# Optimization experiments

Measured on AMD Instinct MI355X. Metric: run time of the kernel, lower is better.

The kernel has to match this reference:

```python
import jax, jax.numpy as jnp
import numpy as np
from jax.scipy.special import logsumexp

REG = 1.0
N_ITER = 50  # fixed Sinkhorn iterations (log-domain, stabilized)


def setup_inputs() -> dict:
    key = jax.random.key(0)
    k1, k2 = jax.random.split(key)
    source = jax.random.normal(k1, (8192, 256), dtype=jnp.float32)
    target = jax.random.normal(k2, (8192, 256), dtype=jnp.float32)
    return {"source": source, "target": target}


def _sinkhorn_value(x, y, reg):
    # squared euclidean cost matrix [n, m]
    M = (jnp.sum(x * x, axis=1)[:, None]
         + jnp.sum(y * y, axis=1)[None, :]
         - 2.0 * (x @ y.T))
    n, m = M.shape
    loga = -jnp.log(jnp.float32(n))  # uniform weights
    logb = -jnp.log(jnp.float32(m))
    Mr = M / reg

    def step(fg, _):
        f, g = fg
        # f_i = -reg * logsumexp_j((g_j - M_ij)/reg + log b_j)
        f = -reg * logsumexp(g[None, :] / reg - Mr + logb, axis=1)
        g = -reg * logsumexp(f[:, None] / reg - Mr + loga, axis=0)
        return (f, g), None

    f0 = jnp.zeros((n,), dtype=M.dtype)
    g0 = jnp.zeros((m,), dtype=M.dtype)
    (f, g), _ = jax.lax.scan(step, (f0, g0), None, length=N_ITER)

    # log P_ij = (f_i + g_j - M_ij)/reg + log a_i + log b_j
    logP = (f[:, None] + g[None, :]) / reg - Mr + (loga + logb)
    P = jnp.exp(logP)
    value_linear = jnp.sum(P * M)
    # KL(P || a x b) entropic term (reg_type='KL' default in POT)
    kl = jnp.sum(P * (logP - loga - logb))
    return value_linear + reg * kl


def reference(source, target):
    value = _sinkhorn_value(source, target, REG)
    return jnp.sqrt(value)
```

## Files before the change

### kernel.cpp

```cpp
#include <hip/hip_runtime.h>

#define N 8192
#define DK 256
#define LOG2E 1.4426950408889634f
#define LN2   0.6931471805599453f
#define ZS    2.5f
#define QS    1.1541560327f
#define BIAS  320.0f

typedef unsigned short u16;
typedef u16   ushort8 __attribute__((ext_vector_type(8)));
typedef __bf16 bf16x8 __attribute__((ext_vector_type(8)));
typedef float  f32x4  __attribute__((ext_vector_type(4)));

__device__ __forceinline__ u16 f2bf(float f){
  unsigned u = __builtin_bit_cast(unsigned, f);
  return (u16)((u + 0x7fffu + ((u >> 16) & 1u)) >> 16);
}
__device__ __forceinline__ float ex2(float x){
  float r; asm("v_exp_f32 %0, %1" : "=v"(r) : "v"(x)); return r;
}
__device__ __forceinline__ float lg2(float x){
  float r; asm("v_log_f32 %0, %1" : "=v"(r) : "v"(x)); return r;
}
__device__ __forceinline__ float cub0(unsigned u){ float r; asm("v_cvt_f32_ubyte0 %0, %1":"=v"(r):"v"(u)); return r; }
__device__ __forceinline__ float cub1(unsigned u){ float r; asm("v_cvt_f32_ubyte1 %0, %1":"=v"(r):"v"(u)); return r; }
__device__ __forceinline__ float cub2(unsigned u){ float r; asm("v_cvt_f32_ubyte2 %0, %1":"=v"(r):"v"(u)); return r; }
__device__ __forceinline__ float cub3(unsigned u){ float r; asm("v_cvt_f32_ubyte3 %0, %1":"=v"(r):"v"(u)); return r; }

__device__ __forceinline__ float quad(unsigned u, float4 gv, float M){
  float t0 = __builtin_fmaf(cub0(u), ZS, gv.x - M);
  float t1 = __builtin_fmaf(cub1(u), ZS, gv.y - M);
  float t2 = __builtin_fmaf(cub2(u), ZS, gv.z - M);
  float t3 = __builtin_fmaf(cub3(u), ZS, gv.w - M);
  return (ex2(t0) + ex2(t1)) + (ex2(t2) + ex2(t3));
}

__global__ __launch_bounds__(256) void prep_k(const float* __restrict__ x, const float* __restrict__ y,
                                              u16* __restrict__ xb, u16* __restrict__ yb,
                                              float* __restrict__ x2, float* __restrict__ y2,
                                              float* __restrict__ gts){
  const int w = threadIdx.x >> 6, l = threadIdx.x & 63;
  const int r = blockIdx.x * 4 + w;
  const bool isx = r < N;
  const int rr = isx ? r : r - N;
  const float* src = (isx ? x : y) + (size_t)rr * DK;
  float4 v = *(const float4*)(src + l * 4);
  ushort4 bv;
  bv.x = f2bf(v.x); bv.y = f2bf(v.y); bv.z = f2bf(v.z); bv.w = f2bf(v.w);
  *(ushort4*)((isx ? xb : yb) + (size_t)rr * DK + l * 4) = bv;
  float p = v.x*v.x + v.y*v.y + v.z*v.z + v.w*v.w;
  #pragma unroll
  for (int off = 32; off > 0; off >>= 1) p += __shfl_down(p, off);
  if (l == 0){
    if (isx) x2[rr] = p;
    else { y2[rr] = p; gts[rr] = -p * LOG2E - BIAS; }
  }
}

__global__ __launch_bounds__(256) void gemm_k(const u16* __restrict__ xb, const u16* __restrict__ yb,
                                              unsigned char* __restrict__ zq,
                                              unsigned char* __restrict__ zqT){
  __shared__ __align__(16) u16 As[128 * 72];
  __shared__ __align__(16) u16 Bs[128 * 72];
  const int t = threadIdx.x;
  const int w = t >> 6, l = t & 63;
  const int wm = w >> 1, wn = w & 1;
  const int brow = blockIdx.y * 128, bcol = blockIdx.x * 128;
  const int tr = t >> 3, tc = t & 7;
  f32x4 acc[4][4] = {};
  for (int ks = 0; ks < 4; ++ks){
    #pragma unroll
    for (int rr = 0; rr < 4; ++rr){
      const int row = tr + rr * 32;
      *(ushort8*)&As[row * 72 + tc * 8] = *(const ushort8*)&xb[(size_t)(brow + row) * DK + ks * 64 + tc * 8];
      *(ushort8*)&Bs[row * 72 + tc * 8] = *(const ushort8*)&yb[(size_t)(bcol + row) * DK + ks * 64 + tc * 8];
    }
    __syncthreads();
    #pragma unroll
    for (int kk = 0; kk < 2; ++kk){
      bf16x8 av[4], bv[4];
      #pragma unroll
      for (int mi = 0; mi < 4; ++mi){
        const int ar = wm * 64 + mi * 16 + (l & 15);
        av[mi] = __builtin_bit_cast(bf16x8, *(const ushort8*)&As[ar * 72 + kk * 32 + (l >> 4) * 8]);
      }
      #pragma unroll
      for (int ni = 0; ni < 4; ++ni){
        const int br = wn * 64 + ni * 16 + (l & 15);
        bv[ni] = __builtin_bit_cast(bf16x8, *(const ushort8*)&Bs[br * 72 + kk * 32 + (l >> 4) * 8]);
      }
      #pragma unroll
      for (int mi = 0; mi < 4; ++mi)
        #pragma unroll
        for (int ni = 0; ni < 4; ++ni)
          acc[mi][ni] = __builtin_amdgcn_mfma_f32_16x16x32_bf16(av[mi], bv[ni], acc[mi][ni], 0, 0, 0);
    }
    __syncthreads();
  }
  unsigned char* Cs = (unsigned char*)As;
  unsigned char* Ct = (unsigned char*)Bs;
  #pragma unroll
  for (int mi = 0; mi < 4; ++mi){
    const int rowb = wm * 64 + mi * 16 + (l >> 4) * 4;
    #pragma unroll
    for (int ni = 0; ni < 4; ++ni){
      const int col = wn * 64 + ni * 16 + (l & 15);
      unsigned pk = 0;
      #pragma unroll
      for (int rr = 0; rr < 4; ++rr){
        float q = fminf(fmaxf(acc[mi][ni][rr] * QS, -127.f), 127.f);
        unsigned b = (unsigned)((int)__builtin_rintf(q) + 128) & 255u;
        Cs[(rowb + rr) * 128 + col] = (unsigned char)b;
        pk |= b << (8 * rr);
      }
      *(unsigned*)(Ct + col * 144 + rowb) = pk;
    }
  }
  __syncthreads();
  const int trow0 = t >> 3, kseg = t & 7;
  #pragma unroll
  for (int ii = 0; ii < 4; ++ii){
    const int row = trow0 + ii * 32;
    int4 v = *(const int4*)(Cs + row * 128 + kseg * 16);
    *(int4*)(zq + (size_t)(brow + row) * N + bcol + kseg * 16) = v;
    int4 vt = *(const int4*)(Ct + row * 144 + kseg * 16);
    *(int4*)(zqT + (size_t)(bcol + row) * N + brow + kseg * 16) = vt;
  }
}

__global__ __launch_bounds__(256) void sweept_k(const unsigned char* __restrict__ z,
                                                const float* __restrict__ din,
                                                float* __restrict__ dout,
                                                float* __restrict__ pmax_out){
  const int w = threadIdx.x >> 6, l = threadIdx.x & 63;
  const int i = blockIdx.x * 4 + w;
  const unsigned char* zr = z + (size_t)i * N + l * 16;
  float m = -1e30f, s = 0.f;
  uint4 zA = *(const uint4*)(zr);
  #pragma unroll
  for (int it = 0; it < 8; ++it){
    uint4 zB = zA;
    if (it < 7) zB = *(const uint4*)(zr + (it + 1) * 1024);
    const float* gp = din + it * 1024 + l * 16;
    const float4 g0 = *(const float4*)(gp);
    const float4 g1 = *(const float4*)(gp + 4);
    const float4 g2 = *(const float4*)(gp + 8);
    const float4 g3 = *(const float4*)(gp + 12);
    float tt[16];
    tt[0]  = __builtin_fmaf(cub0(zA.x), ZS, g0.x);
    tt[1]  = __builtin_fmaf(cub1(zA.x), ZS, g0.y);
    tt[2]  = __builtin_fmaf(cub2(zA.x), ZS, g0.z);
    tt[3]  = __builtin_fmaf(cub3(zA.x), ZS, g0.w);
    tt[4]  = __builtin_fmaf(cub0(zA.y), ZS, g1.x);
    tt[5]  = __builtin_fmaf(cub1(zA.y), ZS, g1.y);
    tt[6]  = __builtin_fmaf(cub2(zA.y), ZS, g1.z);
    tt[7]  = __builtin_fmaf(cub3(zA.y), ZS, g1.w);
    tt[8]  = __builtin_fmaf(cub0(zA.z), ZS, g2.x);
    tt[9]  = __builtin_fmaf(cub1(zA.z), ZS, g2.y);
    tt[10] = __builtin_fmaf(cub2(zA.z), ZS, g2.z);
    tt[11] = __builtin_fmaf(cub3(zA.z), ZS, g2.w);
    tt[12] = __builtin_fmaf(cub0(zA.w), ZS, g3.x);
    tt[13] = __builtin_fmaf(cub1(zA.w), ZS, g3.y);
    tt[14] = __builtin_fmaf(cub2(zA.w), ZS, g3.z);
    tt[15] = __builtin_fmaf(cub3(zA.w), ZS, g3.w);
    float a0 = fmaxf(tt[0], tt[1]),  a1 = fmaxf(tt[2], tt[3]);
    float a2 = fmaxf(tt[4], tt[5]),  a3 = fmaxf(tt[6], tt[7]);
    float a4 = fmaxf(tt[8], tt[9]),  a5 = fmaxf(tt[10], tt[11]);
    float a6 = fmaxf(tt[12], tt[13]), a7 = fmaxf(tt[14], tt[15]);
    float b0 = fmaxf(a0, a1), b1 = fmaxf(a2, a3), b2 = fmaxf(a4, a5), b3 = fmaxf(a6, a7);
    float nm = fmaxf(fmaxf(fmaxf(b0, b1), fmaxf(b2, b3)), m);
    float s0 = ex2(tt[0] - nm) + ex2(tt[1] - nm) + ex2(tt[2] - nm) + ex2(tt[3] - nm)
             + ex2(tt[4] - nm) + ex2(tt[5] - nm) + ex2(tt[6] - nm) + ex2(tt[7] - nm);
    float s1 = ex2(tt[8] - nm) + ex2(tt[9] - nm) + ex2(tt[10] - nm) + ex2(tt[11] - nm)
             + ex2(tt[12] - nm) + ex2(tt[13] - nm) + ex2(tt[14] - nm) + ex2(tt[15] - nm);
    s = __builtin_fmaf(s, ex2(m - nm), s0 + s1);
    m = nm;
    zA = zB;
  }
  #pragma unroll
  for (int off = 32; off > 0; off >>= 1){
    float om = __shfl_down(m, off);
    float os = __shfl_down(s, off);
    float nm = fmaxf(m, om);
    s = __builtin_fmaf(s, ex2(m - nm), os * ex2(om - nm));
    m = nm;
  }
  if (l == 0){
    float lse2 = m + lg2(s);
    dout[i] = 13.0f - lse2 - BIAS;
    pmax_out[i] = lse2;
  }
}

template<int MODE>
__global__ __launch_bounds__(256) void sweepn_k(const unsigned char* __restrict__ z,
                                                const float* __restrict__ din,
                                                float* __restrict__ dout,
                                                const float* __restrict__ pmax_in,
                                                float* __restrict__ pmax_out,
                                                const float* __restrict__ fprev,
                                                const float* __restrict__ x2,
                                                float* __restrict__ contrib){
  __shared__ __align__(16) float gl[8192];
  const int t = threadIdx.x;
  #pragma unroll
  for (int i = 0; i < 8; ++i){
    const int idx = (t + i * 256) * 4;
    *(float4*)(gl + idx) = *(const float4*)(din + idx);
  }
  __syncthreads();
  const int w = t >> 6, l = t & 63;
  const int r0 = blockIdx.x * 8 + w * 2;
  const unsigned char* zr = z + (size_t)r0 * N + l * 16;
  const float M0 = pmax_in[r0], M1 = pmax_in[r0 + 1];
  float s0 = 0.f, s1 = 0.f;
  #pragma unroll 2
  for (int it = 0; it < 8; ++it){
    const uint4 a = *(const uint4*)(zr + it * 1024);
    const uint4 b = *(const uint4*)(zr + N + it * 1024);
    const int cb = it * 1024 + l * 16;
    {
      const float4 gv = *(const float4*)(gl + cb);
      s0 += quad(a.x, gv, M0); s1 += quad(b.x, gv, M1);
    }
    {
      const float4 gv = *(const float4*)(gl + cb + 4);
      s0 += quad(a.y, gv, M0); s1 += quad(b.y, gv, M1);
    }
    {
      const float4 gv = *(const float4*)(gl + cb + 8);
      s0 += quad(a.z, gv, M0); s1 += quad(b.z, gv, M1);
    }
    {
      const float4 gv = *(const float4*)(gl + cb + 12);
      s0 += quad(a.w, gv, M0); s1 += quad(b.w, gv, M1);
    }
  }
  #pragma unroll
  for (int off = 32; off > 0; off >>= 1){
    s0 += __shfl_down(s0, off);
    s1 += __shfl_down(s1, off);
  }
  if (l == 0){
    const float lse0 = M0 + lg2(s0);
    const float lse1 = M1 + lg2(s1);
    if (MODE == 0){
      dout[r0]     = 13.0f - lse0 - BIAS;
      dout[r0 + 1] = 13.0f - lse1 - BIAS;
      pmax_out[r0]     = lse0;
      pmax_out[r0 + 1] = lse1;
    } else {
      const float f0 = fprev[r0] + BIAS;
      const float f1 = fprev[r0 + 1] + BIAS;
      contrib[r0]     = (f0 * LN2 + x2[r0])     * ex2(f0 + lse0 - 26.0f);
      contrib[r0 + 1] = (f1 * LN2 + x2[r0 + 1]) * ex2(f1 + lse1 - 26.0f);
    }
  }
}

__global__ __launch_bounds__(256) void finish_k(const float* __restrict__ contrib,
                                                const float* __restrict__ gts,
                                                const float* __restrict__ y2,
                                                float* __restrict__ out){
  __shared__ float s1[256], s2[256];
  const int t = threadIdx.x;
  float a = 0.f, b = 0.f;
  for (int j = t; j < N; j += 256){ a += contrib[j]; b += (gts[j] + BIAS) * LN2 + y2[j]; }
  s1[t] = a; s2[t] = b; __syncthreads();
  for (int st = 128; st > 0; st >>= 1){
    if (t < st){ s1[t] += s1[t + st]; s2[t] += s2[t + st]; }
    __syncthreads();
  }
  if (t == 0) out[0] = sqrtf(s1[0] + s2[0] * (1.0f / (float)N));
}

extern "C" void kernel_launch(void* const* d_in, const int* in_sizes, int n_in,
                              void* d_out, int out_size, void* d_ws, size_t ws_size,
                              hipStream_t stream){
  const float* x = (const float*)d_in[0];
  const float* y = (const float*)d_in[1];
  float* out = (float*)d_out;
  char* ws = (char*)d_ws;

  unsigned char* zq  = (unsigned char*)(ws);
  unsigned char* zqT = (unsigned char*)(ws + 67108864);
  u16*   xb      = (u16*)  (ws + 134217728);
  u16*   yb      = (u16*)  (ws + 138412032);
  float* x2      = (float*)(ws + 142606336);
  float* y2      = (float*)(ws + 142639104);
  float* fts     = (float*)(ws + 142671872);
  float* gts     = (float*)(ws + 142704640);
  float* contrib = (float*)(ws + 142737408);
  float* pmaxF   = (float*)(ws + 142770176);
  float* pmaxG   = (float*)(ws + 142802944);

  prep_k<<<4096, 256, 0, stream>>>(x, y, xb, yb, x2, y2, gts);
  gemm_k<<<dim3(64, 64), 256, 0, stream>>>(xb, yb, zq, zqT);
  for (int it = 0; it < 2; ++it){
    sweept_k<<<2048, 256, 0, stream>>>(zq,  gts, fts, pmaxF);
    sweept_k<<<2048, 256, 0, stream>>>(zqT, fts, gts, pmaxG);
  }
  for (int s = 4; s < 100; ++s){
    if ((s & 1) == 0)
      sweepn_k<0><<<1024, 256, 0, stream>>>(zq,  gts, fts, pmaxF, pmaxF,
                                            nullptr, nullptr, nullptr);
    else
      sweepn_k<0><<<1024, 256, 0, stream>>>(zqT, fts, gts, pmaxG, pmaxG,
                                            nullptr, nullptr, nullptr);
  }
  sweepn_k<1><<<1024, 256, 0, stream>>>(zq, gts, nullptr, pmaxF, nullptr,
                                        fts, x2, contrib);
  finish_k<<<1, 256, 0, stream>>>(contrib, gts, y2, out);
}
```

Baseline: 1.708 ms.

## Fuse all Sinkhorn sweeps into one persistent cooperative kernel with grid sync

Replaces about 100 separate sweep kernel launches plus the value and finish kernels with one cooperative persistent kernel of 256 blocks × 512 threads. It uses grid.sync between half-iterations and stages the dual vector in LDS on each step. This removes per-launch overhead and the tail idle time between dependent launches. In exchange it adds grid-wide barrier cost, lowers parallelism from 1024 blocks to 256, and each block now handles 32 rows. The old multi-kernel path stays as a fallback if the cooperative launch fails.

```diff
diff --git a/kernel.cpp b/kernel.cpp
--- a/kernel.cpp
+++ b/kernel.cpp
@@ -1,4 +1,7 @@
 #include <hip/hip_runtime.h>
+#include <hip/hip_cooperative_groups.h>
+
+namespace cg = cooperative_groups;
 
 #define N 8192
 #define DK 256
@@ -34,6 +37,48 @@
   float t2 = __builtin_fmaf(cub2(u), ZS, gv.z - M);
   float t3 = __builtin_fmaf(cub3(u), ZS, gv.w - M);
   return (ex2(t0) + ex2(t1)) + (ex2(t2) + ex2(t3));
+}
+__device__ __forceinline__ float pm16(const uint4 a, const float* gp, float M){
+  const float4 g0 = *(const float4*)(gp);
+  const float4 g1 = *(const float4*)(gp + 4);
+  const float4 g2 = *(const float4*)(gp + 8);
+  const float4 g3 = *(const float4*)(gp + 12);
+  return (quad(a.x, g0, M) + quad(a.y, g1, M))
+       + (quad(a.z, g2, M) + quad(a.w, g3, M));
+}
+__device__ __forceinline__ void upd16(const uint4 a, const float* gp, float& m, float& s){
+  const float4 g0 = *(const float4*)(gp);
+  const float4 g1 = *(const float4*)(gp + 4);
+  const float4 g2 = *(const float4*)(gp + 8);
+  const float4 g3 = *(const float4*)(gp + 12);
+  float t0  = __builtin_fmaf(cub0(a.x), ZS, g0.x);
+  float t1  = __builtin_fmaf(cub1(a.x), ZS, g0.y);
+  float t2  = __builtin_fmaf(cub2(a.x), ZS, g0.z);
+  float t3  = __builtin_fmaf(cub3(a.x), ZS, g0.w);
+  float t4  = __builtin_fmaf(cub0(a.y), ZS, g1.x);
+  float t5  = __builtin_fmaf(cub1(a.y), ZS, g1.y);
+  float t6  = __builtin_fmaf(cub2(a.y), ZS, g1.z);
+  float t7  = __builtin_fmaf(cub3(a.y), ZS, g1.w);
+  float t8  = __builtin_fmaf(cub0(a.z), ZS, g2.x);
+  float t9  = __builtin_fmaf(cub1(a.z), ZS, g2.y);
+  float t10 = __builtin_fmaf(cub2(a.z), ZS, g2.z);
+  float t11 = __builtin_fmaf(cub3(a.z), ZS, g2.w);
+  float t12 = __builtin_fmaf(cub0(a.w), ZS, g3.x);
+  float t13 = __builtin_fmaf(cub1(a.w), ZS, g3.y);
+  float t14 = __builtin_fmaf(cub2(a.w), ZS, g3.z);
+  float t15 = __builtin_fmaf(cub3(a.w), ZS, g3.w);
+  float a0 = fmaxf(t0, t1),   a1 = fmaxf(t2, t3);
+  float a2 = fmaxf(t4, t5),   a3 = fmaxf(t6, t7);
+  float a4 = fmaxf(t8, t9),   a5 = fmaxf(t10, t11);
+  float a6 = fmaxf(t12, t13), a7 = fmaxf(t14, t15);
+  float b0 = fmaxf(a0, a1), b1 = fmaxf(a2, a3), b2 = fmaxf(a4, a5), b3 = fmaxf(a6, a7);
+  float nm = fmaxf(fmaxf(fmaxf(b0, b1), fmaxf(b2, b3)), m);
+  float s0 = ex2(t0 - nm) + ex2(t1 - nm) + ex2(t2 - nm) + ex2(t3 - nm)
+           + ex2(t4 - nm) + ex2(t5 - nm) + ex2(t6 - nm) + ex2(t7 - nm);
+  float s1 = ex2(t8 - nm) + ex2(t9 - nm) + ex2(t10 - nm) + ex2(t11 - nm)
+           + ex2(t12 - nm) + ex2(t13 - nm) + ex2(t14 - nm) + ex2(t15 - nm);
+  s = __builtin_fmaf(s, ex2(m - nm), s0 + s1);
+  m = nm;
 }
 
 __global__ __launch_bounds__(256) void prep_k(const float* __restrict__ x, const float* __restrict__ y,
@@ -129,6 +174,147 @@
   }
 }
 
+template<int PHASE>
+__device__ __forceinline__ void do_pair(const unsigned char* __restrict__ z,
+                                        const float* gl, int r0, int l,
+                                        float* __restrict__ dout,
+                                        float* __restrict__ pmax){
+  const unsigned char* zr = z + (size_t)r0 * N + l * 16;
+  float lse0, lse1;
+  if (PHASE == 0){
+    float m0 = -1e30f, s0 = 0.f, m1 = -1e30f, s1 = 0.f;
+    #pragma unroll 2
+    for (int it = 0; it < 8; ++it){
+      const uint4 a = *(const uint4*)(zr + it * 1024);
+      const uint4 b = *(const uint4*)(zr + N + it * 1024);
+      const float* gp = gl + it * 1024 + l * 16;
+      upd16(a, gp, m0, s0);
+      upd16(b, gp, m1, s1);
+    }
+    #pragma unroll
+    for (int off = 32; off > 0; off >>= 1){
+      float om = __shfl_down(m0, off), os = __shfl_down(s0, off);
+      float nm = fmaxf(m0, om);
+      s0 = __builtin_fmaf(s0, ex2(m0 - nm), os * ex2(om - nm)); m0 = nm;
+      om = __shfl_down(m1, off); os = __shfl_down(s1, off);
+      nm = fmaxf(m1, om);
+      s1 = __builtin_fmaf(s1, ex2(m1 - nm), os * ex2(om - nm)); m1 = nm;
+    }
+    lse0 = m0 + lg2(s0); lse1 = m1 + lg2(s1);
+  } else {
+    const float M0 = pmax[r0], M1 = pmax[r0 + 1];
+    float s0 = 0.f, s1 = 0.f;
+    #pragma unroll 2
+    for (int it = 0; it < 8; ++it){
+      const uint4 a = *(const uint4*)(zr + it * 1024);
+      const uint4 b = *(const uint4*)(zr + N + it * 1024);
+      const float* gp = gl + it * 1024 + l * 16;
+      s0 += pm16(a, gp, M0);
+      s1 += pm16(b, gp, M1);
+    }
+    #pragma unroll
+    for (int off = 32; off > 0; off >>= 1){
+      s0 += __shfl_down(s0, off);
+      s1 += __shfl_down(s1, off);
+    }
+    lse0 = M0 + lg2(s0); lse1 = M1 + lg2(s1);
+  }
+  if (l == 0){
+    dout[r0]     = 13.0f - lse0 - BIAS;
+    dout[r0 + 1] = 13.0f - lse1 - BIAS;
+    pmax[r0]     = lse0;
+    pmax[r0 + 1] = lse1;
+  }
+}
+
+__device__ __forceinline__ void val_pair(const unsigned char* __restrict__ zq,
+                                         const float* gl, int r0, int l,
+                                         const float* __restrict__ pmaxF,
+                                         const float* __restrict__ fts,
+                                         const float* __restrict__ x2,
+                                         float* __restrict__ contrib){
+  const unsigned char* zr = zq + (size_t)r0 * N + l * 16;
+  const float M0 = pmaxF[r0], M1 = pmaxF[r0 + 1];
+  float s0 = 0.f, s1 = 0.f;
+  #pragma unroll 2
+  for (int it = 0; it < 8; ++it){
+    const uint4 a = *(const uint4*)(zr + it * 1024);
+    const uint4 b = *(const uint4*)(zr + N + it * 1024);
+    const float* gp = gl + it * 1024 + l * 16;
+    s0 += pm16(a, gp, M0);
+    s1 += pm16(b, gp, M1);
+  }
+  #pragma unroll
+  for (int off = 32; off > 0; off >>= 1){
+    s0 += __shfl_down(s0, off);
+    s1 += __shfl_down(s1, off);
+  }
+  if (l == 0){
+    const float lse0 = M0 + lg2(s0), lse1 = M1 + lg2(s1);
+    const float f0 = fts[r0] + BIAS, f1 = fts[r0 + 1] + BIAS;
+    contrib[r0]     = (f0 * LN2 + x2[r0])     * ex2(f0 + lse0 - 26.0f);
+    contrib[r0 + 1] = (f1 * LN2 + x2[r0 + 1]) * ex2(f1 + lse1 - 26.0f);
+  }
+}
+
+__global__ __launch_bounds__(512, 2) void sink_k(
+    const unsigned char* __restrict__ zq, const unsigned char* __restrict__ zqT,
+    float* __restrict__ fts, float* __restrict__ gts,
+    float* __restrict__ pmaxF, float* __restrict__ pmaxG,
+    const float* __restrict__ x2, const float* __restrict__ y2,
+    float* __restrict__ contrib, float* __restrict__ out){
+  cg::grid_group grid = cg::this_grid();
+  __shared__ __align__(16) float gl[8192];
+  const int t = threadIdx.x;
+  const int w = t >> 6, l = t & 63;
+  const int rA = blockIdx.x * 32 + w * 2;
+  const int rB = rA + 16;
+  for (int s = 0; s < 100; ++s){
+    const bool fs = !(s & 1);
+    const unsigned char* z = fs ? zq : zqT;
+    const float* din = fs ? gts : fts;
+    float* dout = fs ? fts : gts;
+    float* pmax = fs ? pmaxF : pmaxG;
+    #pragma unroll
+    for (int i = 0; i < 4; ++i){
+      const int idx = (t + i * 512) * 4;
+      *(float4*)(gl + idx) = *(const float4*)(din + idx);
+    }
+    __syncthreads();
+    if (s < 4){
+      do_pair<0>(z, gl, rA, l, dout, pmax);
+      do_pair<0>(z, gl, rB, l, dout, pmax);
+    } else {
+      do_pair<1>(z, gl, rA, l, dout, pmax);
+      do_pair<1>(z, gl, rB, l, dout, pmax);
+    }
+    grid.sync();
+  }
+  #pragma unroll
+  for (int i = 0; i < 4; ++i){
+    const int idx = (t + i * 512) * 4;
+    *(float4*)(gl + idx) = *(const float4*)(gts + idx);
+  }
+  __syncthreads();
+  val_pair(zq, gl, rA, l, pmaxF, fts, x2, contrib);
+  val_pair(zq, gl, rB, l, pmaxF, fts, x2, contrib);
+  grid.sync();
+  if (blockIdx.x == 0){
+    float a = 0.f, b = 0.f;
+    for (int j = t; j < N; j += 512){
+      a += contrib[j];
+      b += (gts[j] + BIAS) * LN2 + y2[j];
+    }
+    gl[t] = a; gl[512 + t] = b;
+    __syncthreads();
+    for (int st = 256; st > 0; st >>= 1){
+      if (t < st){ gl[t] += gl[t + st]; gl[512 + t] += gl[512 + t + st]; }
+      __syncthreads();
+    }
+    if (t == 0) out[0] = sqrtf(gl[0] + gl[512] * (1.0f / (float)N));
+  }
+}
+
 __global__ __launch_bounds__(256) void sweept_k(const unsigned char* __restrict__ z,
                                                 const float* __restrict__ din,
                                                 float* __restrict__ dout,
@@ -137,46 +323,10 @@
   const int i = blockIdx.x * 4 + w;
   const unsigned char* zr = z + (size_t)i * N + l * 16;
   float m = -1e30f, s = 0.f;
-  uint4 zA = *(const uint4*)(zr);
-  #pragma unroll
+  #pragma unroll 2
   for (int it = 0; it < 8; ++it){
-    uint4 zB = zA;
-    if (it < 7) zB = *(const uint4*)(zr + (it + 1) * 1024);
-    const float* gp = din + it * 1024 + l * 16;
-    const float4 g0 = *(const float4*)(gp);
-    const float4 g1 = *(const float4*)(gp + 4);
-    const float4 g2 = *(const float4*)(gp + 8);
-    const float4 g3 = *(const float4*)(gp + 12);
-    float tt[16];
-    tt[0]  = __builtin_fmaf(cub0(zA.x), ZS, g0.x);
-    tt[1]  = __builtin_fmaf(cub1(zA.x), ZS, g0.y);
-    tt[2]  = __builtin_fmaf(cub2(zA.x), ZS, g0.z);
-    tt[3]  = __builtin_fmaf(cub3(zA.x), ZS, g0.w);
-    tt[4]  = __builtin_fmaf(cub0(zA.y), ZS, g1.x);
-    tt[5]  = __builtin_fmaf(cub1(zA.y), ZS, g1.y);
-    tt[6]  = __builtin_fmaf(cub2(zA.y), ZS, g1.z);
-    tt[7]  = __builtin_fmaf(cub3(zA.y), ZS, g1.w);
-    tt[8]  = __builtin_fmaf(cub0(zA.z), ZS, g2.x);
-    tt[9]  = __builtin_fmaf(cub1(zA.z), ZS, g2.y);
-    tt[10] = __builtin_fmaf(cub2(zA.z), ZS, g2.z);
-    tt[11] = __builtin_fmaf(cub3(zA.z), ZS, g2.w);
-    tt[12] = __builtin_fmaf(cub0(zA.w), ZS, g3.x);
-    tt[13] = __builtin_fmaf(cub1(zA.w), ZS, g3.y);
-    tt[14] = __builtin_fmaf(cub2(zA.w), ZS, g3.z);
-    tt[15] = __builtin_fmaf(cub3(zA.w), ZS, g3.w);
-    float a0 = fmaxf(tt[0], tt[1]),  a1 = fmaxf(tt[2], tt[3]);
-    float a2 = fmaxf(tt[4], tt[5]),  a3 = fmaxf(tt[6], tt[7]);
-    float a4 = fmaxf(tt[8], tt[9]),  a5 = fmaxf(tt[10], tt[11]);
-    float a6 = fmaxf(tt[12], tt[13]), a7 = fmaxf(tt[14], tt[15]);
-    float b0 = fmaxf(a0, a1), b1 = fmaxf(a2, a3), b2 = fmaxf(a4, a5), b3 = fmaxf(a6, a7);
-    float nm = fmaxf(fmaxf(fmaxf(b0, b1), fmaxf(b2, b3)), m);
-    float s0 = ex2(tt[0] - nm) + ex2(tt[1] - nm) + ex2(tt[2] - nm) + ex2(tt[3] - nm)
-             + ex2(tt[4] - nm) + ex2(tt[5] - nm) + ex2(tt[6] - nm) + ex2(tt[7] - nm);
-    float s1 = ex2(tt[8] - nm) + ex2(tt[9] - nm) + ex2(tt[10] - nm) + ex2(tt[11] - nm)
-             + ex2(tt[12] - nm) + ex2(tt[13] - nm) + ex2(tt[14] - nm) + ex2(tt[15] - nm);
-    s = __builtin_fmaf(s, ex2(m - nm), s0 + s1);
-    m = nm;
-    zA = zB;
+    const uint4 zA = *(const uint4*)(zr + it * 1024);
+    upd16(zA, din + it * 1024 + l * 16, m, s);
   }
   #pragma unroll
   for (int off = 32; off > 0; off >>= 1){
@@ -219,23 +369,9 @@
   for (int it = 0; it < 8; ++it){
     const uint4 a = *(const uint4*)(zr + it * 1024);
     const uint4 b = *(const uint4*)(zr + N + it * 1024);
-    const int cb = it * 1024 + l * 16;
-    {
-      const float4 gv = *(const float4*)(gl + cb);
-      s0 += quad(a.x, gv, M0); s1 += quad(b.x, gv, M1);
-    }
-    {
-      const float4 gv = *(const float4*)(gl + cb + 4);
-      s0 += quad(a.y, gv, M0); s1 += quad(b.y, gv, M1);
-    }
-    {
-      const float4 gv = *(const float4*)(gl + cb + 8);
-      s0 += quad(a.z, gv, M0); s1 += quad(b.z, gv, M1);
-    }
-    {
-      const float4 gv = *(const float4*)(gl + cb + 12);
-      s0 += quad(a.w, gv, M0); s1 += quad(b.w, gv, M1);
-    }
+    const float* gp = gl + it * 1024 + l * 16;
+    s0 += pm16(a, gp, M0);
+    s1 += pm16(b, gp, M1);
   }
   #pragma unroll
   for (int off = 32; off > 0; off >>= 1){
@@ -297,19 +433,28 @@
 
   prep_k<<<4096, 256, 0, stream>>>(x, y, xb, yb, x2, y2, gts);
   gemm_k<<<dim3(64, 64), 256, 0, stream>>>(xb, yb, zq, zqT);
-  for (int it = 0; it < 2; ++it){
-    sweept_k<<<2048, 256, 0, stream>>>(zq,  gts, fts, pmaxF);
-    sweept_k<<<2048, 256, 0, stream>>>(zqT, fts, gts, pmaxG);
-  }
-  for (int s = 4; s < 100; ++s){
-    if ((s & 1) == 0)
-      sweepn_k<0><<<1024, 256, 0, stream>>>(zq,  gts, fts, pmaxF, pmaxF,
-                                            nullptr, nullptr, nullptr);
-    else
-      sweepn_k<0><<<1024, 256, 0, stream>>>(zqT, fts, gts, pmaxG, pmaxG,
-                                            nullptr, nullptr, nullptr);
-  }
-  sweepn_k<1><<<1024, 256, 0, stream>>>(zq, gts, nullptr, pmaxF, nullptr,
-                                        fts, x2, contrib);
-  finish_k<<<1, 256, 0, stream>>>(contrib, gts, y2, out);
-}
+
+  void* args[] = { (void*)&zq, (void*)&zqT, (void*)&fts, (void*)&gts,
+                   (void*)&pmaxF, (void*)&pmaxG, (void*)&x2, (void*)&y2,
+                   (void*)&contrib, (void*)&out };
+  hipError_t err = hipLaunchCooperativeKernel((const void*)sink_k,
+                                              dim3(256), dim3(512),
+                                              args, 0, stream);
+  if (err != hipSuccess){
+    for (int it = 0; it < 2; ++it){
+      sweept_k<<<2048, 256, 0, stream>>>(zq,  gts, fts, pmaxF);
+      sweept_k<<<2048, 256, 0, stream>>>(zqT, fts, gts, pmaxG);
+    }
+    for (int s = 4; s < 100; ++s){
+      if ((s & 1) == 0)
+        sweepn_k<0><<<1024, 256, 0, stream>>>(zq,  gts, fts, pmaxF, pmaxF,
+                                              nullptr, nullptr, nullptr);
+      else
+        sweepn_k<0><<<1024, 256, 0, stream>>>(zqT, fts, gts, pmaxG, pmaxG,
+                                              nullptr, nullptr, nullptr);
+    }
+    sweepn_k<1><<<1024, 256, 0, stream>>>(zq, gts, nullptr, pmaxF, nullptr,
+                                          fts, x2, contrib);
+    finish_k<<<1, 256, 0, stream>>>(contrib, gts, y2, out);
+  }
+}
```

Measured after the change: 4.584 ms. +168.4%, slower.
